# Kernel tuning notes

Measured on AMD Instinct MI355X. Metric: run time of the kernel, lower is better.

## Reference

```python
import jax, jax.numpy as jnp
import numpy as np

B, S, H = 32, 512, 768
NHEAD, DH = 8, 96          # 8 heads * 96 = 768
E = 4096                   # edges per sample
NC = 2
NEG = -1e9
EPS = 1e-5


def _p(k, shape, scale=0.02):
    return scale * jax.random.normal(k, shape, dtype=jnp.float32)


def setup_inputs() -> dict:
    key = jax.random.key(0)
    ks = jax.random.split(key, 24)
    z = lambda *s: jnp.zeros(s, jnp.float32)
    return {
        "diff_encoded": jax.random.normal(ks[0], (B, S, H), jnp.float32),
        "msg_encoded": jax.random.normal(ks[1], (B, S, H), jnp.float32),
        "msg_mask": jnp.ones((B, S), jnp.int32),
        "edge_index_diff": jax.random.randint(ks[2], (B, 2, E), 0, S),
        "edge_index_msg": jax.random.randint(ks[3], (B, 2, E), 0, S),
        # GATv2Conv(heads=1): lin_l (source/message), lin_r (target), att vector, output bias
        "gat_wl": _p(ks[4], (H, H)), "gat_bl": z(H),
        "gat_wr": _p(ks[5], (H, H)), "gat_br": z(H),
        "gat_att": _p(ks[6], (H,)), "gat_bias": z(H),
        # cross MultiheadAttention
        "wq": _p(ks[7], (H, H)), "bq": z(H),
        "wk": _p(ks[8], (H, H)), "bk": z(H),
        "wv": _p(ks[9], (H, H)), "bv": z(H),
        "wo": _p(ks[10], (H, H)), "bo": z(H),
        # LayerNorm + MLP head
        "ln_g": jnp.ones((H,), jnp.float32), "ln_b": z(H),
        "fc0_w": _p(ks[11], (H, 512)), "fc0_b": z(512),
        "fc1_w": _p(ks[12], (512, 128)), "fc1_b": z(128),
        "fc2_w": _p(ks[13], (128, NC)), "fc2_b": z(NC),
    }


def _gat_single(x, edges, wl, bl, wr, br, att, bias):
    # GATv2Conv, heads=1, add_self_loops=True. x: [N,H], edges: [2,E] (src, dst).
    N = x.shape[0]
    src, dst = edges[0], edges[1]
    valid = (src < N) & (dst < N)            # clip_edge_index, as a mask
    src = jnp.where(valid, src, 0)
    dst = jnp.where(valid, dst, 0)
    loop = jnp.arange(N, dtype=src.dtype)    # PyG adds self loops
    src_a = jnp.concatenate([src, loop])
    dst_a = jnp.concatenate([dst, loop])
    valid_a = jnp.concatenate([valid, jnp.ones((N,), bool)])
    xl = x @ wl + bl                          # source / message transform
    xr = x @ wr + br                          # target transform
    e = jax.nn.leaky_relu(xl[src_a] + xr[dst_a], 0.2) @ att   # [E+N]
    e = jnp.where(valid_a, e, NEG)
    emax = jax.ops.segment_max(e, dst_a, num_segments=N)
    p = jnp.exp(e - emax[dst_a]) * valid_a.astype(x.dtype)
    denom = jax.ops.segment_sum(p, dst_a, num_segments=N)
    alpha = p / denom[dst_a]
    out = jax.ops.segment_sum(alpha[:, None] * xl[src_a], dst_a, num_segments=N)
    return out + bias


_gat = jax.vmap(_gat_single, in_axes=(0, 0) + (None,) * 6)


def _layernorm(x, g, b):
    mu = jnp.mean(x, -1, keepdims=True)
    var = jnp.mean(jnp.square(x - mu), -1, keepdims=True)
    return (x - mu) * jax.lax.rsqrt(var + EPS) * g + b


def reference(diff_encoded, msg_encoded, msg_mask, edge_index_diff, edge_index_msg,
              gat_wl, gat_bl, gat_wr, gat_br, gat_att, gat_bias,
              wq, bq, wk, bk, wv, bv, wo, bo, ln_g, ln_b,
              fc0_w, fc0_b, fc1_w, fc1_b, fc2_w, fc2_b):
    diff_g = _gat(diff_encoded, edge_index_diff, gat_wl, gat_bl, gat_wr, gat_br, gat_att, gat_bias) + diff_encoded
    msg_g = _gat(msg_encoded, edge_index_msg, gat_wl, gat_bl, gat_wr, gat_br, gat_att, gat_bias) + msg_encoded
    # cross attention: query=diff_g, key/value=msg_g, key_padding_mask = (msg_mask == 0)
    q = (diff_g @ wq + bq).reshape(B, S, NHEAD, DH)
    k = (msg_g @ wk + bk).reshape(B, S, NHEAD, DH)
    v = (msg_g @ wv + bv).reshape(B, S, NHEAD, DH)
    scores = jnp.einsum("bqhd,bkhd->bhqk", q, k) / jnp.sqrt(jnp.float32(DH))
    scores = jnp.where((msg_mask == 0)[:, None, None, :], NEG, scores)
    attn = jax.nn.softmax(scores, axis=-1)
    ctx = jnp.einsum("bhqk,bkhd->bqhd", attn, v).reshape(B, S, H) @ wo + bo
    fused = _layernorm(ctx + diff_g, ln_g, ln_b)
    x = fused[:, 0, :]                                  # CLS token
    x = jax.nn.relu(x @ fc0_w + fc0_b)                  # dropout = identity (eval)
    x = jax.nn.relu(x @ fc1_w + fc1_b)
    return x @ fc2_w + fc2_b
```

## Files before the change

### kernel.cpp

```cpp
#include <hip/hip_runtime.h>
#include <hip/hip_bf16.h>
#include <math.h>

#define BB 32
#define SS 512
#define HH 768
#define NHEADC 8
#define DHC 96
#define EE 4096
#define NCC 2
#define CAPC 128
#define CAP2 32
#define GSL 36
#define NEGV -1000000000.0f
#define EPSV 1e-5f

#define PREP_CVT  12288
#define PREP_WT   2304
#define PREP_BIAS 3
#define PREP_CNT  512
#define PREP_TOT  (PREP_CVT + PREP_WT + PREP_BIAS + PREP_CNT)

typedef __hip_bfloat16 bf16;
typedef __bf16 bf16x8 __attribute__((ext_vector_type(8)));
typedef float f32x4 __attribute__((ext_vector_type(4)));

static __device__ inline unsigned short f2bf_u(float f) {
  __hip_bfloat16 h = __float2bfloat16(f);
  return *(unsigned short*)&h;
}
static __device__ inline float bfu(unsigned short u) {
  return __uint_as_float(((unsigned int)u) << 16);
}
static __device__ inline float bf2f(bf16 h) { return __bfloat162float(h); }

static __device__ inline void gload16(const void* g, void* l) {
  __builtin_amdgcn_global_load_lds(
      (const __attribute__((address_space(1))) void*)g,
      (__attribute__((address_space(3))) void*)l, 16, 0, 0);
}

__global__ __launch_bounds__(256) void k_prep(
    const float* __restrict__ msg_enc, bf16* __restrict__ Abf,
    const float* __restrict__ gat_wl, const float* __restrict__ gat_wr,
    const float* __restrict__ wk, const float* __restrict__ wv,
    bf16* __restrict__ wtA, bf16* __restrict__ wtB,
    const float* __restrict__ gat_bl, const float* __restrict__ gat_br,
    const float* __restrict__ bk, const float* __restrict__ bv,
    float* __restrict__ biasA, float* __restrict__ biasB,
    const int* __restrict__ e_msg, const int* __restrict__ e_diff,
    int* __restrict__ cnt, int* __restrict__ dcnt, int* __restrict__ dsrc)
{
  int blk = blockIdx.x, tid = threadIdx.x;
  if (blk < PREP_CVT) {
    int i = (blk * 256 + tid) * 4;
    float4 v = *(const float4*)(msg_enc + i);
    ushort4 o;
    o.x = f2bf_u(v.x); o.y = f2bf_u(v.y); o.z = f2bf_u(v.z); o.w = f2bf_u(v.w);
    *(ushort4*)((unsigned short*)Abf + i) = o;
    return;
  }
  blk -= PREP_CVT;
  if (blk < PREP_WT) {
    int z = blk / 576, rr = blk - z * 576;
    int bx = rr % 24, by = rr / 24;
    const float* w; bf16* o;
    switch (z) {
      case 0: w = gat_wl; o = wtA; break;
      case 1: w = gat_wr; o = wtA + (size_t)HH * HH; break;
      case 2: w = wk;     o = wtB; break;
      default: w = wv;    o = wtB + (size_t)HH * HH; break;
    }
    __shared__ float t[32][33];
    int n0 = bx * 32, k0 = by * 32;
    int x = tid & 31, y = tid >> 5;
    for (int yy = y; yy < 32; yy += 8)
      t[yy][x] = w[(size_t)(k0 + yy) * HH + n0 + x];
    __syncthreads();
    for (int yy = y; yy < 32; yy += 8)
      o[(size_t)(n0 + yy) * HH + k0 + x] = __float2bfloat16(t[x][yy]);
    return;
  }
  blk -= PREP_WT;
  if (blk < PREP_BIAS) {
    int t = blk * 256 + tid;
    if (t < HH) {
      biasA[t] = gat_bl[t]; biasA[HH + t] = gat_br[t];
      biasB[t] = bk[t];     biasB[HH + t] = bv[t];
    }
    return;
  }
  blk -= PREP_BIAS;
  {
    int i = blk * 256 + tid;
    if (i >= BB * EE) return;
    int b = i / EE, j = i - b * EE;
    int s = e_msg[b * 2 * EE + j], d = e_msg[b * 2 * EE + EE + j];
    if (s >= 0 && s < SS && d >= 0 && d < SS)
      atomicAdd(&cnt[b * SS + d], 1);
    int s2 = e_diff[b * 2 * EE + j], d2 = e_diff[b * 2 * EE + EE + j];
    if (s2 >= 0 && s2 < SS && d2 == 0) {
      int pos = atomicAdd(&dcnt[b], 1);
      if (pos < CAPC) dsrc[b * CAPC + pos] = s2;
    }
    if (j == 0) {
      int pos = atomicAdd(&dcnt[b], 1);
      if (pos < CAPC) dsrc[b * CAPC + pos] = 0;
    }
  }
}

template <typename OT>
__global__ __launch_bounds__(256) void k_gemm(
    const bf16* __restrict__ A, const bf16* __restrict__ Bt,
    const float* __restrict__ bias, OT* __restrict__ C0, OT* __restrict__ C1,
    int M, int K)
{
  __shared__ __align__(16) bf16 As0[128 * 32];
  __shared__ __align__(16) bf16 As1[128 * 32];
  __shared__ __align__(16) bf16 Bs0[128 * 32];
  __shared__ __align__(16) bf16 Bs1[128 * 32];
  const int tid = threadIdx.x;
  const int wv = tid >> 6, lane = tid & 63;
  const int bm = blockIdx.x * 128, bn = blockIdx.y * 128;
  const int wm = (wv & 1) * 64, wn = (wv >> 1) * 64;
  const int m16 = lane & 15, half = lane >> 4;
  f32x4 acc[4][4];
  #pragma unroll
  for (int i = 0; i < 4; ++i)
    #pragma unroll
    for (int j = 0; j < 4; ++j) acc[i][j] = (f32x4){0.f, 0.f, 0.f, 0.f};

  const int c0 = tid, c1 = tid + 256;
  const int r0 = c0 >> 2, o0 = (c0 & 3) * 8;
  const int r1 = c1 >> 2, o1 = (c1 & 3) * 8;
  const size_t aB0 = (size_t)(bm + r0) * K + o0;
  const size_t aB1 = (size_t)(bm + r1) * K + o1;
  const size_t bB0 = (size_t)(bn + r0) * K + o0;
  const size_t bB1 = (size_t)(bn + r1) * K + o1;

  for (int k0 = 0; k0 < K; k0 += 64) {
    __syncthreads();
    gload16(A + aB0 + k0, As0 + (size_t)c0 * 8);
    gload16(A + aB1 + k0, As0 + (size_t)c1 * 8);
    gload16(A + aB0 + k0 + 32, As1 + (size_t)c0 * 8);
    gload16(A + aB1 + k0 + 32, As1 + (size_t)c1 * 8);
    gload16(Bt + bB0 + k0, Bs0 + (size_t)c0 * 8);
    gload16(Bt + bB1 + k0, Bs0 + (size_t)c1 * 8);
    gload16(Bt + bB0 + k0 + 32, Bs1 + (size_t)c0 * 8);
    gload16(Bt + bB1 + k0 + 32, Bs1 + (size_t)c1 * 8);
    __syncthreads();
    #pragma unroll
    for (int ks = 0; ks < 2; ++ks) {
      const bf16* Ah = ks ? As1 : As0;
      const bf16* Bh = ks ? Bs1 : Bs0;
      bf16x8 af[4], bfv[4];
      #pragma unroll
      for (int t = 0; t < 4; ++t) {
        af[t]  = *(const bf16x8*)(Ah + (wm + t * 16 + m16) * 32 + half * 8);
        bfv[t] = *(const bf16x8*)(Bh + (wn + t * 16 + m16) * 32 + half * 8);
      }
      #pragma unroll
      for (int i = 0; i < 4; ++i)
        #pragma unroll
        for (int j = 0; j < 4; ++j)
          acc[i][j] = __builtin_amdgcn_mfma_f32_16x16x32_bf16(af[i], bfv[j], acc[i][j], 0, 0, 0);
    }
  }
  #pragma unroll
  for (int i = 0; i < 4; ++i) {
    #pragma unroll
    for (int j = 0; j < 4; ++j) {
      int col = bn + wn + j * 16 + m16;
      float bv = bias ? bias[col] : 0.f;
      OT* Cb = (col < HH) ? C0 : C1;
      int cc = (col < HH) ? col : col - HH;
      #pragma unroll
      for (int r = 0; r < 4; ++r) {
        int row = bm + wm + i * 16 + half * 4 + r;
        float v = acc[i][j][r] + bv;
        if constexpr (sizeof(OT) == 2)
          Cb[(size_t)row * HH + cc] = (OT)__float2bfloat16(v);
        else
          Cb[(size_t)row * HH + cc] = v;
      }
    }
  }
}

__global__ __launch_bounds__(512) void k_scan(const int* __restrict__ cnt,
                                              int* __restrict__ offs,
                                              int* __restrict__ cursor) {
  __shared__ int tmp[SS];
  int b = blockIdx.x, t = threadIdx.x;
  int x = cnt[b * SS + t];
  tmp[t] = x;
  __syncthreads();
  for (int off = 1; off < SS; off <<= 1) {
    int u = (t >= off) ? tmp[t - off] : 0;
    __syncthreads();
    tmp[t] += u;
    __syncthreads();
  }
  int ex = tmp[t] - x;
  offs[b * SS + t] = ex;
  cursor[b * SS + t] = ex;
}

__global__ void k_scatter(const int* __restrict__ e_msg, int* __restrict__ cursor,
                          int* __restrict__ binned) {
  int i = blockIdx.x * blockDim.x + threadIdx.x;
  if (i >= BB * EE) return;
  int b = i / EE, j = i - b * EE;
  int s = e_msg[b * 2 * EE + j], d = e_msg[b * 2 * EE + EE + j];
  if (s >= 0 && s < SS && d >= 0 && d < SS) {
    int pos = atomicAdd(&cursor[b * SS + d], 1);
    binned[(size_t)b * EE + pos] = s;
  }
}

__global__ __launch_bounds__(256) void k_gat_fused(
    const int* __restrict__ binned, const int* __restrict__ offs,
    const int* __restrict__ cnt, const bf16* __restrict__ xl,
    const bf16* __restrict__ xrb, const float* __restrict__ att,
    const float* __restrict__ gbias, const bf16* __restrict__ resid,
    bf16* __restrict__ out)
{
  int bid = blockIdx.x;
  int xcd = bid & 7, idx = bid >> 3;
  int b = xcd * 4 + (idx >> 7);
  int d = (idx & 127) * 4 + (threadIdx.x >> 6);
  int lane = threadIdx.x & 63;
  int base = offs[b * SS + d], n = cnt[b * SS + d];
  const int* bin = binned + (size_t)b * EE + base;
  float av[12];
  {
    const float4* a4 = (const float4*)att;
    #pragma unroll
    for (int r = 0; r < 3; ++r) {
      float4 t = a4[lane + 64 * r];
      av[4*r] = t.x; av[4*r+1] = t.y; av[4*r+2] = t.z; av[4*r+3] = t.w;
    }
  }
  float xr[12];
  {
    const ushort4* p = (const ushort4*)(xrb + ((size_t)b * SS + d) * HH);
    #pragma unroll
    for (int r = 0; r < 3; ++r) {
      ushort4 v = p[lane + 64 * r];
      xr[4*r] = bfu(v.x); xr[4*r+1] = bfu(v.y); xr[4*r+2] = bfu(v.z); xr[4*r+3] = bfu(v.w);
    }
  }
  float m = -3.0e38f, l = 0.f;
  float acc[12] = {};
  int nn = n + 1;
  ushort4 pre[3];
  {
    const ushort4* p = (const ushort4*)(xl + ((size_t)b * SS + d) * HH);
    pre[0] = p[lane]; pre[1] = p[lane + 64]; pre[2] = p[lane + 128];
  }
  for (int j = 0; j < nn; ++j) {
    ushort4 cur0 = pre[0], cur1 = pre[1], cur2 = pre[2];
    if (j + 1 < nn) {
      int sn = bin[j];
      const ushort4* p = (const ushort4*)(xl + ((size_t)b * SS + sn) * HH);
      pre[0] = p[lane]; pre[1] = p[lane + 64]; pre[2] = p[lane + 128];
    }
    float xs[12];
    xs[0] = bfu(cur0.x); xs[1] = bfu(cur0.y); xs[2]  = bfu(cur0.z); xs[3]  = bfu(cur0.w);
    xs[4] = bfu(cur1.x); xs[5] = bfu(cur1.y); xs[6]  = bfu(cur1.z); xs[7]  = bfu(cur1.w);
    xs[8] = bfu(cur2.x); xs[9] = bfu(cur2.y); xs[10] = bfu(cur2.z); xs[11] = bfu(cur2.w);
    float e = 0.f;
    #pragma unroll
    for (int k = 0; k < 12; ++k) {
      float t = xs[k] + xr[k];
      t = t > 0.f ? t : 0.2f * t;
      e += t * av[k];
    }
    #pragma unroll
    for (int off = 32; off > 0; off >>= 1) e += __shfl_xor(e, off);
    float mn = fmaxf(m, e);
    float so = __expf(m - mn);
    float w  = __expf(e - mn);
    l = l * so + w;
    #pragma unroll
    for (int k = 0; k < 12; ++k) acc[k] = acc[k] * so + w * xs[k];
    m = mn;
  }
  float inv = 1.f / l;
  size_t o = ((size_t)b * SS + d) * HH;
  const float4* gb4 = (const float4*)gbias;
  const ushort4* rs4 = (const ushort4*)(resid + o);
  ushort4* out4 = (ushort4*)(out + o);
  #pragma unroll
  for (int r = 0; r < 3; ++r) {
    int c = lane + 64 * r;
    float4 gg = gb4[c];
    ushort4 rr = rs4[c];
    ushort4 ov;
    ov.x = f2bf_u(acc[4*r+0] * inv + gg.x + bfu(rr.x));
    ov.y = f2bf_u(acc[4*r+1] * inv + gg.y + bfu(rr.y));
    ov.z = f2bf_u(acc[4*r+2] * inv + gg.z + bfu(rr.z));
    ov.w = f2bf_u(acc[4*r+3] * inv + gg.w + bfu(rr.w));
    out4[c] = ov;
  }
}

__global__ __launch_bounds__(192) void k_gather_diff(
    const int* __restrict__ dcnt, const int* __restrict__ dsrc,
    const float* __restrict__ diff_enc, bf16* __restrict__ G)
{
  int b = blockIdx.y, jj = blockIdx.x;
  int n = min(dcnt[b], CAP2);
  int t = threadIdx.x;
  size_t orow = ((size_t)b * GSL + jj) * HH;
  ushort4 o = {0, 0, 0, 0};
  if (jj < n || jj == CAP2) {
    int s = (jj == CAP2) ? 0 : dsrc[b * CAPC + jj];
    float4 v = ((const float4*)(diff_enc + ((size_t)b * SS + s) * HH))[t];
    o.x = f2bf_u(v.x); o.y = f2bf_u(v.y); o.z = f2bf_u(v.z); o.w = f2bf_u(v.w);
  }
  *(ushort4*)((unsigned short*)G + orow + t * 4) = o;
}

__global__ __launch_bounds__(256) void k_diff_gat0(
    const int* __restrict__ dcnt, const float* __restrict__ GDl,
    const float* __restrict__ GDr, const float* __restrict__ att,
    const float* __restrict__ gbias, const float* __restrict__ diff_enc,
    float* __restrict__ dg0)
{
  int b = blockIdx.x;
  int n = min(dcnt[b], CAP2);
  __shared__ float ee[CAP2];
  __shared__ float al[CAP2];
  __shared__ float xr0s[HH];
  int wave = threadIdx.x >> 6, lane = threadIdx.x & 63;
  for (int h = threadIdx.x; h < HH; h += 256)
    xr0s[h] = GDr[((size_t)b * GSL + CAP2) * HH + h];
  __syncthreads();
  for (int jj = wave; jj < n; jj += 4) {
    const float* px = GDl + ((size_t)b * GSL + jj) * HH;
    float part = 0.f;
    #pragma unroll
    for (int r = 0; r < HH / 64; ++r) {
      int h = lane + 64 * r;
      float t = px[h] + xr0s[h];
      t = t > 0.f ? t : 0.2f * t;
      part += t * att[h];
    }
    #pragma unroll
    for (int off = 32; off > 0; off >>= 1) part += __shfl_xor(part, off);
    if (lane == 0) ee[jj] = part;
  }
  __syncthreads();
  if (threadIdx.x == 0) {
    float m = -3.0e38f;
    for (int i = 0; i < n; ++i) m = fmaxf(m, ee[i]);
    float ssum = 0.f;
    for (int i = 0; i < n; ++i) ssum += expf(ee[i] - m);
    float inv = 1.f / ssum;
    for (int i = 0; i < n; ++i) al[i] = expf(ee[i] - m) * inv;
  }
  __syncthreads();
  for (int h = threadIdx.x; h < HH; h += 256) {
    float acc = 0.f;
    for (int i = 0; i < n; ++i) acc += al[i] * GDl[((size_t)b * GSL + i) * HH + h];
    dg0[b * HH + h] = acc + gbias[h] + diff_enc[(size_t)b * SS * HH + h];
  }
}

__global__ __launch_bounds__(256) void k_colmat(
    const float* __restrict__ in, const float* __restrict__ w,
    const float* __restrict__ bias, const float* __restrict__ extra,
    float* __restrict__ outp, int Kd, int Nd, long in_stride, int relu)
{
  int b = blockIdx.y, n0 = blockIdx.x * 64;
  int tid = threadIdx.x, wv = tid >> 6, lane = tid & 63;
  __shared__ float xs[HH];
  __shared__ float red[4][64];
  const float* src = in + (size_t)b * in_stride;
  for (int k = tid; k < Kd; k += 256) xs[k] = src[k];
  __syncthreads();
  int h = n0 + lane;
  int kpw = Kd >> 2;
  int kb = wv * kpw;
  float acc = 0.f;
  for (int k = 0; k < kpw; k += 8) {
    #pragma unroll
    for (int u = 0; u < 8; ++u) {
      int kk = kb + k + u;
      acc += xs[kk] * w[(size_t)kk * Nd + h];
    }
  }
  red[wv][lane] = acc;
  __syncthreads();
  if (tid < 64) {
    float s = red[0][tid] + red[1][tid] + red[2][tid] + red[3][tid] + bias[n0 + tid];
    if (extra) s += extra[(size_t)b * Nd + n0 + tid];
    if (relu) s = fmaxf(s, 0.f);
    outp[(size_t)b * Nd + n0 + tid] = s;
  }
}

__global__ __launch_bounds__(256) void k_ln(
    const float* __restrict__ xin, const float* __restrict__ g,
    const float* __restrict__ bta, float* __restrict__ yout)
{
  int b = blockIdx.x, tid = threadIdx.x;
  __shared__ float red[4], redq[4];
  float v0 = xin[b * HH + tid];
  float v1 = xin[b * HH + tid + 256];
  float v2 = xin[b * HH + tid + 512];
  float sum = v0 + v1 + v2;
  float sq = v0 * v0 + v1 * v1 + v2 * v2;
  #pragma unroll
  for (int off = 32; off > 0; off >>= 1) { sum += __shfl_xor(sum, off); sq += __shfl_xor(sq, off); }
  int wv = tid >> 6, lane = tid & 63;
  if (lane == 0) { red[wv] = sum; redq[wv] = sq; }
  __syncthreads();
  sum = red[0] + red[1] + red[2] + red[3];
  sq = redq[0] + redq[1] + redq[2] + redq[3];
  float mu = sum / HH;
  float var = sq / HH - mu * mu;
  float scl = rsqrtf(var + EPSV);
  yout[b * HH + tid]       = (v0 - mu) * scl * g[tid]       + bta[tid];
  yout[b * HH + tid + 256] = (v1 - mu) * scl * g[tid + 256] + bta[tid + 256];
  yout[b * HH + tid + 512] = (v2 - mu) * scl * g[tid + 512] + bta[tid + 512];
}

__global__ __launch_bounds__(256) void k_fc12(
    const float* __restrict__ a0g, const float* __restrict__ fc1w,
    const float* __restrict__ fc1b, const float* __restrict__ fc2w,
    const float* __restrict__ fc2b, float* __restrict__ out)
{
  int b = blockIdx.x, tid = threadIdx.x;
  __shared__ float a0s[512];
  __shared__ float a1s[128];
  __shared__ float r1[2][128];
  for (int k = tid; k < 512; k += 256) a0s[k] = a0g[b * 512 + k];
  __syncthreads();
  int o = tid & 127, hf = tid >> 7;
  int kb = hf * 256;
  float acc = 0.f;
  for (int k = 0; k < 256; k += 8) {
    #pragma unroll
    for (int u = 0; u < 8; ++u) {
      int kk = kb + k + u;
      acc += a0s[kk] * fc1w[(size_t)kk * 128 + o];
    }
  }
  r1[hf][o] = acc;
  __syncthreads();
  if (tid < 128) a1s[tid] = fmaxf(r1[0][tid] + r1[1][tid] + fc1b[tid], 0.f);
  __syncthreads();
  if (tid < 128) {
    int oo = tid >> 6, l = tid & 63;
    float p = a1s[l] * fc2w[l * 2 + oo] + a1s[l + 64] * fc2w[(l + 64) * 2 + oo];
    #pragma unroll
    for (int off = 32; off > 0; off >>= 1) p += __shfl_xor(p, off);
    if (l == 0) out[b * NCC + oo] = p + fc2b[oo];
  }
}

__global__ __launch_bounds__(512) void k_attn(
    const float* __restrict__ q0, const bf16* __restrict__ kb,
    const bf16* __restrict__ vb, const int* __restrict__ mask,
    float* __restrict__ ctx)
{
  int b = blockIdx.x / NHEADC, hd = blockIdx.x % NHEADC;
  __shared__ float qs[DHC];
  __shared__ float sc[SS];
  __shared__ float redm[8];
  __shared__ float reds[8];
  __shared__ float pr4[4][DHC];
  int tid = threadIdx.x;
  if (tid < DHC) qs[tid] = q0[b * HH + hd * DHC + tid];
  __syncthreads();
  const float scale = 0.10206207261596575f;
  {
    int s = tid;
    const int4* pk4 = (const int4*)(kb + ((size_t)b * SS + s) * HH + hd * DHC);
    float acc = 0.f;
    #pragma unroll
    for (int c = 0; c < 12; ++c) {
      int4 raw = pk4[c];
      const unsigned short* u = (const unsigned short*)&raw;
      #pragma unroll
      for (int j = 0; j < 8; ++j) acc += qs[c * 8 + j] * bfu(u[j]);
    }
    sc[s] = (mask[b * SS + s] != 0) ? acc * scale : NEGV;
  }
  __syncthreads();
  int wave = tid >> 6, lane = tid & 63;
  float m = sc[tid];
  #pragma unroll
  for (int off = 32; off > 0; off >>= 1) m = fmaxf(m, __shfl_xor(m, off));
  if (lane == 0) redm[wave] = m;
  __syncthreads();
  m = redm[0];
  #pragma unroll
  for (int i = 1; i < 8; ++i) m = fmaxf(m, redm[i]);
  float p0 = expf(sc[tid] - m);
  float ssum = p0;
  #pragma unroll
  for (int off = 32; off > 0; off >>= 1) ssum += __shfl_xor(ssum, off);
  if (lane == 0) reds[wave] = ssum;
  __syncthreads();
  ssum = reds[0] + reds[1] + reds[2] + reds[3] + reds[4] + reds[5] + reds[6] + reds[7];
  float inv = 1.f / ssum;
  sc[tid] = p0 * inv;
  __syncthreads();
  {
    int hs = tid >> 7, d = tid & 127;
    if (d < DHC) {
      const bf16* pv = vb + ((size_t)b * SS + hs * 128) * HH + hd * DHC + d;
      float acc = 0.f;
      for (int s = 0; s < 128; s += 8) {
        #pragma unroll
        for (int u = 0; u < 8; ++u)
          acc += sc[hs * 128 + s + u] * bf2f(pv[(size_t)(s + u) * HH]);
      }
      pr4[hs][d] = acc;
    }
  }
  __syncthreads();
  if (tid < DHC)
    ctx[b * HH + hd * DHC + tid] = pr4[0][tid] + pr4[1][tid] + pr4[2][tid] + pr4[3][tid];
}

extern "C" void kernel_launch(void* const* d_in, const int* in_sizes, int n_in,
                              void* d_out, int out_size, void* d_ws, size_t ws_size,
                              hipStream_t stream) {
  const float* diff_enc = (const float*)d_in[0];
  const float* msg_enc  = (const float*)d_in[1];
  const int*   msg_mask = (const int*)d_in[2];
  const int*   e_diff   = (const int*)d_in[3];
  const int*   e_msg    = (const int*)d_in[4];
  const float* gat_wl   = (const float*)d_in[5];
  const float* gat_bl   = (const float*)d_in[6];
  const float* gat_wr   = (const float*)d_in[7];
  const float* gat_br   = (const float*)d_in[8];
  const float* gat_att  = (const float*)d_in[9];
  const float* gat_bias = (const float*)d_in[10];
  const float* wq = (const float*)d_in[11];
  const float* bq = (const float*)d_in[12];
  const float* wk = (const float*)d_in[13];
  const float* bk = (const float*)d_in[14];
  const float* wv = (const float*)d_in[15];
  const float* bv = (const float*)d_in[16];
  const float* wo = (const float*)d_in[17];
  const float* bo = (const float*)d_in[18];
  const float* ln_g = (const float*)d_in[19];
  const float* ln_b = (const float*)d_in[20];
  const float* fc0w = (const float*)d_in[21];
  const float* fc0b = (const float*)d_in[22];
  const float* fc1w = (const float*)d_in[23];
  const float* fc1b = (const float*)d_in[24];
  const float* fc2w = (const float*)d_in[25];
  const float* fc2b = (const float*)d_in[26];
  float* out = (float*)d_out;

  char* ws = (char*)d_ws;
  size_t off = 0;
  auto alloc = [&](size_t bytes) -> void* {
    void* p = (void*)(ws + off);
    off += (bytes + 255) & ~(size_t)255;
    return p;
  };
  bf16* Abf    = (bf16*)alloc((size_t)BB * SS * HH * 2);
  bf16* xl     = (bf16*)alloc((size_t)BB * SS * HH * 2);
  bf16* xrb    = (bf16*)alloc((size_t)BB * SS * HH * 2);
  bf16* kbuf   = (bf16*)alloc((size_t)BB * SS * HH * 2);
  bf16* vbuf   = (bf16*)alloc((size_t)BB * SS * HH * 2);
  bf16* mg     = (bf16*)alloc((size_t)BB * SS * HH * 2);
  bf16* wtA    = (bf16*)alloc((size_t)2 * HH * HH * 2);
  bf16* wtB    = (bf16*)alloc((size_t)2 * HH * HH * 2);
  float* biasA = (float*)alloc((size_t)2 * HH * 4);
  float* biasB = (float*)alloc((size_t)2 * HH * 4);
  int*   cnt   = (int*)alloc((size_t)BB * SS * 4);
  int*   offs  = (int*)alloc((size_t)BB * SS * 4);
  int*   cursor= (int*)alloc((size_t)BB * SS * 4);
  int*   binned= (int*)alloc((size_t)BB * EE * 4);
  bf16*  G     = (bf16*)alloc((size_t)BB * GSL * HH * 2);
  float* GDl   = (float*)alloc((size_t)BB * GSL * HH * 4);
  float* GDr   = (float*)alloc((size_t)BB * GSL * HH * 4);
  int*   dcnt  = (int*)alloc((size_t)BB * 4);
  int*   dsrc  = (int*)alloc((size_t)BB * CAPC * 4);
  float* dg0   = (float*)alloc((size_t)BB * HH * 4);
  float* q0    = (float*)alloc((size_t)BB * HH * 4);
  float* ctx   = (float*)alloc((size_t)BB * HH * 4);
  float* fpre  = (float*)alloc((size_t)BB * HH * 4);
  float* fnrm  = (float*)alloc((size_t)BB * HH * 4);
  float* a0g   = (float*)alloc((size_t)BB * 512 * 4);

  hipMemsetAsync(cnt, 0, (size_t)BB * SS * 4, stream);
  hipMemsetAsync(dcnt, 0, (size_t)BB * 4, stream);

  k_prep<<<PREP_TOT, 256, 0, stream>>>(msg_enc, Abf, gat_wl, gat_wr, wk, wv,
                                       wtA, wtB, gat_bl, gat_br, bk, bv,
                                       biasA, biasB, e_msg, e_diff,
                                       cnt, dcnt, dsrc);
  k_scan<<<BB, SS, 0, stream>>>(cnt, offs, cursor);
  k_scatter<<<(BB * EE + 255) / 256, 256, 0, stream>>>(e_msg, cursor, binned);

  dim3 gBlk(256), gGridA((BB * SS) / 128, (2 * HH) / 128);
  k_gemm<bf16><<<gGridA, gBlk, 0, stream>>>(Abf, wtA, biasA, xl, xrb, BB * SS, HH);
  k_gat_fused<<<(BB * SS) / 4, 256, 0, stream>>>(binned, offs, cnt, xl, xrb,
                                                 gat_att, gat_bias, Abf, mg);
  k_gemm<bf16><<<gGridA, gBlk, 0, stream>>>(mg, wtB, biasB, kbuf, vbuf, BB * SS, HH);
  {
    dim3 gg(GSL, BB);
    k_gather_diff<<<gg, 192, 0, stream>>>(dcnt, dsrc, diff_enc, G);
    dim3 gGridD((BB * GSL) / 128, (2 * HH) / 128);
    k_gemm<float><<<gGridD, gBlk, 0, stream>>>(G, wtA, biasA, GDl, GDr, BB * GSL, HH);
  }
  k_diff_gat0<<<BB, 256, 0, stream>>>(dcnt, GDl, GDr, gat_att, gat_bias, diff_enc, dg0);
  {
    dim3 g(HH / 64, BB);
    k_colmat<<<g, 256, 0, stream>>>(dg0, wq, bq, nullptr, q0, HH, HH, HH, 0);
  }
  k_attn<<<BB * NHEADC, 512, 0, stream>>>(q0, kbuf, vbuf, msg_mask, ctx);
  {
    dim3 g(HH / 64, BB);
    k_colmat<<<g, 256, 0, stream>>>(ctx, wo, bo, dg0, fpre, HH, HH, HH, 0);
  }
  k_ln<<<BB, 256, 0, stream>>>(fpre, ln_g, ln_b, fnrm);
  {
    dim3 g(512 / 64, BB);
    k_colmat<<<g, 256, 0, stream>>>(fnrm, fc0w, fc0b, nullptr, a0g, HH, 512, HH, 1);
  }
  k_fc12<<<BB, 256, 0, stream>>>(a0g, fc1w, fc1b, fc2w, fc2b, out);
}
```

Measured before the change: 441.0 us.

## Add 256x128-tile triple-buffered bf16 GEMM for the two large projections

Replaces the two large msg GEMMs (16384x1536x768) with a new kernel using 256x128 block tiles, 512 threads, and a three-stage LDS ring with XOR-swizzled async loads. It adds s_setprio around the MFMA groups and remaps block IDs for L2 locality. The aim is more data reuse per block and better overlap of loads with MFMA work, at the cost of more LDS per block (144KB), which limits occupancy.

Measured after the change: 436.1 us. Within noise of the previous version (-1.1%).

```diff
diff --git a/kernel.cpp b/kernel.cpp
--- a/kernel.cpp
+++ b/kernel.cpp
@@ -183,6 +183,142 @@
           Cb[(size_t)row * HH + cc] = (OT)__float2bfloat16(v);
         else
           Cb[(size_t)row * HH + cc] = v;
+      }
+    }
+  }
+}
+
+__global__ __launch_bounds__(512) void k_gemm256(
+    const bf16* __restrict__ A, const bf16* __restrict__ Bt,
+    const float* __restrict__ bias, bf16* __restrict__ C0, bf16* __restrict__ C1)
+{
+  constexpr int K = 768;
+  constexpr int NT = K / 64;
+  __shared__ __align__(16) bf16 Asm[3][256 * 64];
+  __shared__ __align__(16) bf16 Bsm[3][128 * 64];
+
+  const int tid = threadIdx.x;
+  const int wv = tid >> 6, lane = tid & 63;
+  const int m16 = lane & 15, half = lane >> 4;
+
+  const int bid = blockIdx.x;
+  const int swz = (bid & 7) * 96 + (bid >> 3);
+  const int bm = (swz / 12) * 256;
+  const int bn = (swz % 12) * 128;
+
+  const int wm = (wv >> 1) * 64;
+  const int wn = (wv & 1) * 64;
+
+  size_t srcA[4], srcB[2];
+  #pragma unroll
+  for (int li = 0; li < 4; ++li) {
+    int L = li * 512 + tid;
+    int row = L >> 3;
+    int g = (L & 7) ^ (row & 7);
+    srcA[li] = (size_t)(bm + row) * K + g * 8;
+  }
+  #pragma unroll
+  for (int li = 0; li < 2; ++li) {
+    int L = li * 512 + tid;
+    int row = L >> 3;
+    int g = (L & 7) ^ (row & 7);
+    srcB[li] = (size_t)(bn + row) * K + g * 8;
+  }
+
+  auto stage = [&](int t, bf16* ba, bf16* bb) {
+    #pragma unroll
+    for (int li = 0; li < 4; ++li)
+      gload16(A + srcA[li] + (size_t)t * 64, ba + (size_t)(li * 512 + tid) * 8);
+    #pragma unroll
+    for (int li = 0; li < 2; ++li)
+      gload16(Bt + srcB[li] + (size_t)t * 64, bb + (size_t)(li * 512 + tid) * 8);
+  };
+
+  f32x4 acc[4][4];
+  #pragma unroll
+  for (int i = 0; i < 4; ++i)
+    #pragma unroll
+    for (int j = 0; j < 4; ++j) acc[i][j] = (f32x4){0.f, 0.f, 0.f, 0.f};
+
+  const int xr = m16 & 7;
+  const int aoff0 = (wm + m16) * 64 + ((half ^ xr) * 8);
+  const int aoff1 = (wm + m16) * 64 + (((4 + half) ^ xr) * 8);
+  const int boff0 = (wn + m16) * 64 + ((half ^ xr) * 8);
+  const int boff1 = (wn + m16) * 64 + (((4 + half) ^ xr) * 8);
+
+  auto tile = [&](const bf16* __restrict__ Ab, const bf16* __restrict__ Bb) {
+    bf16x8 b0[4], b1[4], a0[2], a1[2], a2[2], a3[2];
+    #pragma unroll
+    for (int j = 0; j < 4; ++j) b0[j] = *(const bf16x8*)(Bb + boff0 + j * 1024);
+    #pragma unroll
+    for (int i = 0; i < 2; ++i) a0[i] = *(const bf16x8*)(Ab + aoff0 + i * 1024);
+    __builtin_amdgcn_s_setprio(1);
+    #pragma unroll
+    for (int i = 0; i < 2; ++i)
+      #pragma unroll
+      for (int j = 0; j < 4; ++j)
+        acc[i][j] = __builtin_amdgcn_mfma_f32_16x16x32_bf16(a0[i], b0[j], acc[i][j], 0, 0, 0);
+    __builtin_amdgcn_s_setprio(0);
+    #pragma unroll
+    for (int i = 0; i < 2; ++i) a1[i] = *(const bf16x8*)(Ab + aoff0 + (i + 2) * 1024);
+    __builtin_amdgcn_s_setprio(1);
+    #pragma unroll
+    for (int i = 0; i < 2; ++i)
+      #pragma unroll
+      for (int j = 0; j < 4; ++j)
+        acc[i + 2][j] = __builtin_amdgcn_mfma_f32_16x16x32_bf16(a1[i], b0[j], acc[i + 2][j], 0, 0, 0);
+    __builtin_amdgcn_s_setprio(0);
+    #pragma unroll
+    for (int j = 0; j < 4; ++j) b1[j] = *(const bf16x8*)(Bb + boff1 + j * 1024);
+    #pragma unroll
+    for (int i = 0; i < 2; ++i) a2[i] = *(const bf16x8*)(Ab + aoff1 + i * 1024);
+    __builtin_amdgcn_s_setprio(1);
+    #pragma unroll
+    for (int i = 0; i < 2; ++i)
+      #pragma unroll
+      for (int j = 0; j < 4; ++j)
+        acc[i][j] = __builtin_amdgcn_mfma_f32_16x16x32_bf16(a2[i], b1[j], acc[i][j], 0, 0, 0);
+    __builtin_amdgcn_s_setprio(0);
+    #pragma unroll
+    for (int i = 0; i < 2; ++i) a3[i] = *(const bf16x8*)(Ab + aoff1 + (i + 2) * 1024);
+    __builtin_amdgcn_s_setprio(1);
+    #pragma unroll
+    for (int i = 0; i < 2; ++i)
+      #pragma unroll
+      for (int j = 0; j < 4; ++j)
+        acc[i + 2][j] = __builtin_amdgcn_mfma_f32_16x16x32_bf16(a3[i], b1[j], acc[i + 2][j], 0, 0, 0);
+    __builtin_amdgcn_s_setprio(0);
+  };
+
+  auto step = [&](int kt, int cur, int nxt) {
+    if (kt == NT - 1) asm volatile("s_waitcnt vmcnt(0)" ::: "memory");
+    else              asm volatile("s_waitcnt vmcnt(6)" ::: "memory");
+    __builtin_amdgcn_s_barrier();
+    __builtin_amdgcn_sched_barrier(0);
+    if (kt + 2 < NT) stage(kt + 2, Asm[nxt], Bsm[nxt]);
+    tile(Asm[cur], Bsm[cur]);
+  };
+
+  stage(0, Asm[0], Bsm[0]);
+  stage(1, Asm[1], Bsm[1]);
+  for (int kt3 = 0; kt3 < NT; kt3 += 3) {
+    step(kt3 + 0, 0, 2);
+    step(kt3 + 1, 1, 0);
+    step(kt3 + 2, 2, 1);
+  }
+
+  #pragma unroll
+  for (int i = 0; i < 4; ++i) {
+    #pragma unroll
+    for (int j = 0; j < 4; ++j) {
+      int col = bn + wn + j * 16 + m16;
+      float bv = bias[col];
+      bf16* Cb = (col < HH) ? C0 : C1;
+      int cc = (col < HH) ? col : col - HH;
+      #pragma unroll
+      for (int r = 0; r < 4; ++r) {
+        int row = bm + wm + i * 16 + half * 4 + r;
+        Cb[(size_t)row * HH + cc] = (bf16)__float2bfloat16(acc[i][j][r] + bv);
       }
     }
   }
@@ -603,12 +739,12 @@
   k_scan<<<BB, SS, 0, stream>>>(cnt, offs, cursor);
   k_scatter<<<(BB * EE + 255) / 256, 256, 0, stream>>>(e_msg, cursor, binned);
 
-  dim3 gBlk(256), gGridA((BB * SS) / 128, (2 * HH) / 128);
-  k_gemm<bf16><<<gGridA, gBlk, 0, stream>>>(Abf, wtA, biasA, xl, xrb, BB * SS, HH);
+  k_gemm256<<<768, 512, 0, stream>>>(Abf, wtA, biasA, xl, xrb);
   k_gat_fused<<<(BB * SS) / 4, 256, 0, stream>>>(binned, offs, cnt, xl, xrb,
                                                  gat_att, gat_bias, Abf, mg);
-  k_gemm<bf16><<<gGridA, gBlk, 0, stream>>>(mg, wtB, biasB, kbuf, vbuf, BB * SS, HH);
-  {
+  k_gemm256<<<768, 512, 0, stream>>>(mg, wtB, biasB, kbuf, vbuf);
+  {
+    dim3 gBlk(256);
     dim3 gg(GSL, BB);
     k_gather_diff<<<gg, 192, 0, stream>>>(dcnt, dsrc, diff_enc, G);
     dim3 gGridD((BB * GSL) / 128, (2 * HH) / 128);
```
